# Performance work log

Measured on AMD Instinct MI355X. Metric: run time of the kernel, lower is better.

## Reference

```python
import jax, jax.numpy as jnp
import numpy as np

F_DIM = 32          # phi_feature_dim
P = 128             # preselection_ap (spatial H=W)
NU = 4              # num_users
N1 = NU - 1         # n_cat1 == n_cat2
N3 = (NU - 1) ** 2  # n_cat3


def setup_inputs() -> dict:
    key = jax.random.key(0)
    k1, k2, k3, k4, k5 = jax.random.split(key, 5)
    B, CIN = 32, 8
    phi_input = jax.random.normal(k1, (B, CIN, P, P), dtype=jnp.float32)
    W1 = jax.random.normal(k2, (4 * F_DIM, CIN), dtype=jnp.float32) * 0.1
    b1 = jax.random.normal(k3, (4 * F_DIM,), dtype=jnp.float32) * 0.1
    W3 = jax.random.normal(k4, (4 * F_DIM, 4 * F_DIM), dtype=jnp.float32) * 0.1
    b3 = jax.random.normal(k5, (4 * F_DIM,), dtype=jnp.float32) * 0.1
    ex = jnp.ones((P, P), dtype=jnp.float32) - jnp.eye(P, dtype=jnp.float32)
    return {"phi_input": phi_input, "W1": W1, "b1": b1, "W3": W3, "b3": b3, "ex": ex}


def _conv1x1(x, W, b):
    # 1x1 conv == channel matmul: [b,c,h,w] x [o,c] -> [b,o,h,w]
    return jnp.einsum('bchw,oc->bohw', x, W) + b[None, :, None, None]


def _postprocess(r, ex):
    f = F_DIM
    c0 = r[:, :f]
    c1 = jnp.einsum('ph,bchw->bcpw', ex, r[:, f:2 * f]) / N1
    c2 = jnp.einsum('bchw,wq->bchq', r[:, 2 * f:3 * f], ex) / N1
    c3 = jnp.einsum('ph,bchw,wq->bcpq', ex, r[:, 3 * f:4 * f], ex) / N3
    return jnp.concatenate((c0, c1, c2, c3), axis=1)


def reference(phi_input, W1, b1, W3, b3, ex):
    r = jax.nn.relu(_conv1x1(phi_input, W1, b1))
    r = _postprocess(r, ex)
    r = jax.nn.relu(_conv1x1(r, W3, b3))
    r = _postprocess(r, ex)
    return r
```

## Files before the change

kernel.cpp:

```cpp
#include <hip/hip_runtime.h>
#include <stdint.h>

#define BATCH 32
#define CIN   8
#define NCH   128
#define PP    128
#define NSTRIP 8
#define KSTRIP 16

typedef __attribute__((ext_vector_type(8))) short    bf16x8;
typedef __attribute__((ext_vector_type(4))) float    f32x4;

__device__ __forceinline__ float bf2f(unsigned short u) {
    union { unsigned int i; float f; } x; x.i = ((unsigned int)u) << 16; return x.f;
}
__device__ __forceinline__ unsigned short f2bf(float f) {
    union { float f; unsigned int i; } x; x.f = f;
    unsigned int r = x.i + 0x7fffu + ((x.i >> 16) & 1u);
    return (unsigned short)(r >> 16);
}
__device__ __forceinline__ unsigned int pk2(float a, float b) {
    return (unsigned int)f2bf(a) | ((unsigned int)f2bf(b) << 16);
}

__device__ __forceinline__ int xcd_swz512(int bid) {
    return (bid & 7) * 64 + (bid >> 3);
}

#define SWZB(row, cb) (((row) << 8) + ((cb) ^ (((row) & 7) << 4)))

__global__ __launch_bounds__(512, 4) void k1_sums(const float* __restrict__ phi,
        const float* __restrict__ W1, const float* __restrict__ b1,
        float* __restrict__ RS1t, float* __restrict__ CS1p) {
    __shared__ float cs_f[128 * 132];
    __shared__ unsigned short phi_b[2][1024];
    int bx = blockIdx.x;
    int b = bx >> 3, strip = bx & 7;
    int p0 = strip * 16;
    int tid = threadIdx.x;
    int wv = tid >> 6, l = tid & 63, lr = l & 15, lg = l >> 4;
    int c0 = wv * 16 + lg * 4;

    bf16x8 w1fr = {0, 0, 0, 0, 0, 0, 0, 0};
    if (lg == 0) {
        int cc = wv * 16 + lr;
        float4 wa = *(const float4*)(W1 + cc * 8);
        float4 wb = *(const float4*)(W1 + cc * 8 + 4);
        w1fr[0] = (short)f2bf(wa.x); w1fr[1] = (short)f2bf(wa.y);
        w1fr[2] = (short)f2bf(wa.z); w1fr[3] = (short)f2bf(wa.w);
        w1fr[4] = (short)f2bf(wb.x); w1fr[5] = (short)f2bf(wb.y);
        w1fr[6] = (short)f2bf(wb.z); w1fr[7] = (short)f2bf(wb.w);
    }
    f32x4 binit = {b1[c0], b1[c0 + 1], b1[c0 + 2], b1[c0 + 3]};
    if (tid < 128) {
        bf16x8 pv;
        #pragma unroll
        for (int ci = 0; ci < 8; ++ci)
            pv[ci] = (short)f2bf(phi[((size_t)(b * CIN + ci) * PP + p0) * PP + tid]);
        *(bf16x8*)(phi_b[0] + tid * 8) = pv;
    }
    __syncthreads();

    f32x4 cs_acc[8];
    #pragma unroll
    for (int i = 0; i < 8; ++i) { f32x4 z = {0.f, 0.f, 0.f, 0.f}; cs_acc[i] = z; }

    int cur = 0;
    for (int r = 0; r < 16; ++r) {
        int p = p0 + r;
        float pfv[8];
        if (r < 15 && tid < 128) {
            #pragma unroll
            for (int ci = 0; ci < 8; ++ci)
                pfv[ci] = phi[((size_t)(b * CIN + ci) * PP + p + 1) * PP + tid];
        }
        const unsigned short* pb = phi_b[cur];
        f32x4 rs4 = {0.f, 0.f, 0.f, 0.f};
        #pragma unroll
        for (int pt = 0; pt < 8; ++pt) {
            int pix = pt * 16 + lr;
            bf16x8 bfr1 = {0, 0, 0, 0, 0, 0, 0, 0};
            if (lg == 0) bfr1 = *(const bf16x8*)(pb + pix * 8);
            f32x4 a = __builtin_amdgcn_mfma_f32_16x16x32_bf16(w1fr, bfr1, binit, 0, 0, 0);
            f32x4 v = {fmaxf(a.x, 0.f), fmaxf(a.y, 0.f), fmaxf(a.z, 0.f), fmaxf(a.w, 0.f)};
            cs_acc[pt] += v;
            rs4 += v;
        }
        #pragma unroll
        for (int m = 1; m < 16; m <<= 1) {
            rs4.x += __shfl_xor(rs4.x, m);
            rs4.y += __shfl_xor(rs4.y, m);
            rs4.z += __shfl_xor(rs4.z, m);
            rs4.w += __shfl_xor(rs4.w, m);
        }
        if (lr == 0)
            *(f32x4*)(RS1t + ((size_t)b * PP + p) * NCH + c0) = rs4;
        if (r < 15 && tid < 128) {
            bf16x8 pv;
            #pragma unroll
            for (int ci = 0; ci < 8; ++ci) pv[ci] = (short)f2bf(pfv[ci]);
            *(bf16x8*)(phi_b[cur ^ 1] + tid * 8) = pv;
        }
        __syncthreads();
        cur ^= 1;
    }
    #pragma unroll
    for (int pt = 0; pt < 8; ++pt) {
        f32x4 v = cs_acc[pt];
        int q = pt * 16 + lr;
        cs_f[(c0 + 0) * 132 + q] = v.x;
        cs_f[(c0 + 1) * 132 + q] = v.y;
        cs_f[(c0 + 2) * 132 + q] = v.z;
        cs_f[(c0 + 3) * 132 + q] = v.w;
    }
    __syncthreads();
    float* dstp = CS1p + (size_t)(b * NSTRIP + strip) * NCH * PP;
    for (int k = tid; k < 16384; k += 512) {
        int cc = k >> 7, q = k & 127;
        dstp[k] = cs_f[cc * 132 + q];
    }
}

__global__ __launch_bounds__(256) void k1b_planes(const float* __restrict__ W3,
        const float* __restrict__ b3, const float* __restrict__ RS1t,
        const float* __restrict__ CS1p, float* __restrict__ Ap,
        float* __restrict__ Bqt, unsigned short* __restrict__ W3bf) {
    int bx = blockIdx.x;
    int b = bx >> 2, og = bx & 3;
    int tid = threadIdx.x;
    __shared__ float cs_g[64][132];
    __shared__ float rs_g[64][132];
    __shared__ float s1_96[32];
    for (int k = tid; k < 64 * 128; k += 256) {
        int r = k >> 7, q = k & 127;
        int ch_c = (r < 32) ? (32 + r) : (64 + r);
        float s = 0.f;
        #pragma unroll
        for (int s8 = 0; s8 < NSTRIP; ++s8)
            s += CS1p[((size_t)(b * NSTRIP + s8) * NCH + ch_c) * PP + q];
        cs_g[r][q] = s;
    }
    for (int k = tid; k < 64 * 128; k += 256) {
        int p = k >> 6, r = k & 63;
        rs_g[r][p] = RS1t[((size_t)b * PP + p) * NCH + 64 + r];
    }
    __syncthreads();
    if (tid < 32) {
        float s = 0.f;
        for (int q = 0; q < 128; ++q) s += cs_g[32 + tid][q];
        s1_96[tid] = s;
    }
    int o = og * 32 + (tid >> 3), qh = tid & 7;
    {
        float wa[64];
        #pragma unroll
        for (int r = 0; r < 64; ++r)
            wa[r] = (r < 32) ? W3[o * NCH + 32 + r] * (1.f / 3.f)
                             : -W3[o * NCH + 64 + r] * (1.f / 9.f);
        #pragma unroll
        for (int j = 0; j < 4; ++j) {
            int q = qh * 16 + j * 4;
            float4 a = {0.f, 0.f, 0.f, 0.f};
            #pragma unroll
            for (int r = 0; r < 64; ++r) {
                float4 cv = *(const float4*)&cs_g[r][q];
                a.x = fmaf(wa[r], cv.x, a.x);
                a.y = fmaf(wa[r], cv.y, a.y);
                a.z = fmaf(wa[r], cv.z, a.z);
                a.w = fmaf(wa[r], cv.w, a.w);
            }
            *(float4*)&Ap[((size_t)b * NCH + o) * PP + q] = a;
        }
    }
    __syncthreads();
    float cc = b3[o];
    #pragma unroll
    for (int r = 0; r < 32; ++r)
        cc = fmaf(W3[o * NCH + 96 + r] * (1.f / 9.f), s1_96[r], cc);
    {
        float wb[64];
        #pragma unroll
        for (int r = 0; r < 64; ++r)
            wb[r] = (r < 32) ? W3[o * NCH + 64 + r] * (1.f / 3.f)
                             : -W3[o * NCH + 64 + r] * (1.f / 9.f);
        #pragma unroll
        for (int j = 0; j < 4; ++j) {
            int p4 = qh * 16 + j * 4;
            float4 a = {0.f, 0.f, 0.f, 0.f};
            #pragma unroll
            for (int r = 0; r < 64; ++r) {
                float4 rv = *(const float4*)&rs_g[r][p4];
                a.x = fmaf(wb[r], rv.x, a.x);
                a.y = fmaf(wb[r], rv.y, a.y);
                a.z = fmaf(wb[r], rv.z, a.z);
                a.w = fmaf(wb[r], rv.w, a.w);
            }
            Bqt[((size_t)b * PP + p4 + 0) * NCH + o] = a.x + cc;
            Bqt[((size_t)b * PP + p4 + 1) * NCH + o] = a.y + cc;
            Bqt[((size_t)b * PP + p4 + 2) * NCH + o] = a.z + cc;
            Bqt[((size_t)b * PP + p4 + 3) * NCH + o] = a.w + cc;
        }
    }
    if (bx == 0) {
        for (int i = 0; i < 16; ++i) {
            int k = tid + i * 256;
            float4 w = *(const float4*)(W3 + k * 4);
            int c0 = (k * 4) & 127;
            float sc = (c0 < 32) ? 1.f : ((c0 < 96) ? (-1.f / 3.f) : (1.f / 9.f));
            unsigned int lo = pk2(w.x * sc, w.y * sc);
            unsigned int hi = pk2(w.z * sc, w.w * sc);
            uint2 u = {lo, hi};
            *(uint2*)(W3bf + k * 4) = u;
        }
    }
}

__global__ __launch_bounds__(512) void k2a_sums(const float* __restrict__ phi,
        const float* __restrict__ W1, const float* __restrict__ b1,
        const unsigned short* __restrict__ W3bf,
        const float* __restrict__ Ap, const float* __restrict__ Bqt,
        float* __restrict__ RSvT, float* __restrict__ CSp) {
    int bx = xcd_swz512(blockIdx.x);
    int b = bx >> 4, strip = bx & 15;
    int p0 = strip * 8;
    __shared__ unsigned short w3_l[16384];
    __shared__ unsigned short t_l[16384];
    __shared__ unsigned short phi_b[2][1024];
    __shared__ float BC_l[2][128];
    __shared__ float rs_part[8][64];
    int tid = threadIdx.x;
    int wv = tid >> 6, l = tid & 63, lr = l & 15, lg = l >> 4;
    int q0 = wv * 16 + lg * 4;
    int c0 = q0;

    #pragma unroll
    for (int i = 0; i < 4; ++i) {
        int k = tid + i * 512;
        int o = k >> 4, cb = (k & 15) * 16;
        bf16x8 v = *(const bf16x8*)(W3bf + k * 8);
        *(bf16x8*)((char*)w3_l + SWZB(o, cb)) = v;
    }
    bf16x8 w1fr = {0, 0, 0, 0, 0, 0, 0, 0};
    if (lg == 0) {
        int cc = wv * 16 + lr;
        float4 wa = *(const float4*)(W1 + cc * 8);
        float4 wb = *(const float4*)(W1 + cc * 8 + 4);
        w1fr[0] = (short)f2bf(wa.x); w1fr[1] = (short)f2bf(wa.y);
        w1fr[2] = (short)f2bf(wa.z); w1fr[3] = (short)f2bf(wa.w);
        w1fr[4] = (short)f2bf(wb.x); w1fr[5] = (short)f2bf(wb.y);
        w1fr[6] = (short)f2bf(wb.z); w1fr[7] = (short)f2bf(wb.w);
    }
    f32x4 binit = {b1[c0], b1[c0 + 1], b1[c0 + 2], b1[c0 + 3]};
    f32x4 apr[6];
    #pragma unroll
    for (int nt = 2; nt < 8; ++nt)
        apr[nt - 2] = *(const f32x4*)(Ap + ((size_t)(b * NCH + nt * 16 + lr)) * PP + q0);
    if (tid < 128) {
        bf16x8 pv;
        #pragma unroll
        for (int ci = 0; ci < 8; ++ci)
            pv[ci] = (short)f2bf(phi[((size_t)(b * CIN + ci) * PP + p0) * PP + tid]);
        *(bf16x8*)(phi_b[0] + tid * 8) = pv;
        BC_l[0][tid] = Bqt[((size_t)b * PP + p0) * NCH + tid];
    }
    __syncthreads();

    f32x4 cs1a = {0.f,0.f,0.f,0.f}, cs1b = {0.f,0.f,0.f,0.f};
    f32x4 cs3a = {0.f,0.f,0.f,0.f}, cs3b = {0.f,0.f,0.f,0.f};

    for (int r = 0; r < 8; ++r) {
        int cur = r & 1, nxt = cur ^ 1;
        int p = p0 + r;
        float pfv[8]; float bcn = 0.f;
        if (r < 7 && tid < 128) {
            #pragma unroll
            for (int ci = 0; ci < 8; ++ci)
                pfv[ci] = phi[((size_t)(b * CIN + ci) * PP + p + 1) * PP + tid];
            bcn = Bqt[((size_t)b * PP + p + 1) * NCH + tid];
        }
        const unsigned short* pb = phi_b[cur];
        #pragma unroll
        for (int pt = 0; pt < 8; ++pt) {
            int pix = pt * 16 + lr;
            bf16x8 bfr1 = {0, 0, 0, 0, 0, 0, 0, 0};
            if (lg == 0) bfr1 = *(const bf16x8*)(pb + pix * 8);
            f32x4 a = __builtin_amdgcn_mfma_f32_16x16x32_bf16(w1fr, bfr1, binit, 0, 0, 0);
            uint2 u;
            u.x = pk2(fmaxf(a.x, 0.f), fmaxf(a.y, 0.f));
            u.y = pk2(fmaxf(a.z, 0.f), fmaxf(a.w, 0.f));
            *(uint2*)((char*)t_l + SWZB(pix, c0 * 2)) = u;
        }
        __syncthreads();
        bf16x8 afr[4];
        #pragma unroll
        for (int ks = 0; ks < 4; ++ks)
            afr[ks] = *(const bf16x8*)((char*)t_l + SWZB(wv * 16 + lr, ks * 64 + lg * 16));
        #pragma unroll
        for (int nt = 2; nt < 8; ++nt) {
            int o = nt * 16 + lr;
            bf16x8 bfr[4];
            #pragma unroll
            for (int ks = 0; ks < 4; ++ks)
                bfr[ks] = *(const bf16x8*)((char*)w3_l + SWZB(o, ks * 64 + lg * 16));
            f32x4 acc = apr[nt - 2] + BC_l[cur][o];
            #pragma unroll
            for (int ks = 0; ks < 4; ++ks)
                acc = __builtin_amdgcn_mfma_f32_16x16x32_bf16(afr[ks], bfr[ks], acc, 0, 0, 0);
            f32x4 v = {fmaxf(acc.x, 0.f), fmaxf(acc.y, 0.f), fmaxf(acc.z, 0.f), fmaxf(acc.w, 0.f)};
            if (nt == 2) cs1a += v;
            else if (nt == 3) cs1b += v;
            else if (nt == 6) cs3a += v;
            else if (nt == 7) cs3b += v;
            if (nt >= 4) {
                float rsv = v.x + v.y + v.z + v.w;
                rsv += __shfl_xor(rsv, 16);
                rsv += __shfl_xor(rsv, 32);
                if (lg == 0) rs_part[wv][(nt - 4) * 16 + lr] = rsv;
            }
        }
        if (r < 7 && tid < 128) {
            bf16x8 pv;
            #pragma unroll
            for (int ci = 0; ci < 8; ++ci) pv[ci] = (short)f2bf(pfv[ci]);
            *(bf16x8*)(phi_b[nxt] + tid * 8) = pv;
            BC_l[nxt][tid] = bcn;
        }
        __syncthreads();
        if (tid < 64) {
            float s = 0.f;
            #pragma unroll
            for (int w8 = 0; w8 < 8; ++w8) s += rs_part[w8][tid];
            RSvT[((size_t)(b * PP + p)) * 64 + tid] = s;
        }
    }
    {
        float* dst = CSp + ((size_t)(b * KSTRIP + strip)) * 64 * PP;
        *(f32x4*)(dst + (size_t)(lr)      * PP + q0) = cs1a;
        *(f32x4*)(dst + (size_t)(16 + lr) * PP + q0) = cs1b;
        *(f32x4*)(dst + (size_t)(32 + lr) * PP + q0) = cs3a;
        *(f32x4*)(dst + (size_t)(48 + lr) * PP + q0) = cs3b;
    }
}

__global__ __launch_bounds__(256) void k2s_reduce(const float* __restrict__ CSp,
        const float* __restrict__ RSvT, float* __restrict__ CSv,
        float* __restrict__ Sb) {
    int bx = blockIdx.x;
    int b = bx >> 3, grp = bx & 7;
    int tid = threadIdx.x;
    #pragma unroll
    for (int it = 0; it < 4; ++it) {
        int idx = grp * 1024 + it * 256 + tid;
        float s = 0.f;
        #pragma unroll
        for (int st = 0; st < KSTRIP; ++st)
            s += CSp[((size_t)(b * KSTRIP + st)) * 64 * PP + idx];
        CSv[(size_t)b * 64 * PP + idx] = s;
    }
    if (grp == 0 && tid < 32) {
        float s = 0.f;
        for (int p = 0; p < PP; ++p) s += RSvT[((size_t)(b * PP + p)) * 64 + 32 + tid];
        Sb[b * 32 + tid] = s;
    }
}

__global__ __launch_bounds__(512) void k2b_out(const float* __restrict__ phi,
        const float* __restrict__ W1, const float* __restrict__ b1,
        const unsigned short* __restrict__ W3bf,
        const float* __restrict__ Ap, const float* __restrict__ Bqt,
        const float* __restrict__ RSvT, const float* __restrict__ CSv,
        const float* __restrict__ Sb, float* __restrict__ out) {
    int bx = xcd_swz512(blockIdx.x);
    int b = bx >> 4, strip = bx & 15;
    int p0 = strip * 8;
    __shared__ unsigned short w3_l[16384];
    __shared__ unsigned short t_l[16384];
    __shared__ unsigned short phi_b[2][1024];
    __shared__ float BC_l[2][128];
    __shared__ float rs_row[2][64];
    int tid = threadIdx.x;
    int wv = tid >> 6, l = tid & 63, lr = l & 15, lg = l >> 4;
    int q0 = wv * 16 + lg * 4;
    int c0 = q0;

    #pragma unroll
    for (int i = 0; i < 4; ++i) {
        int k = tid + i * 512;
        int o = k >> 4, cb = (k & 15) * 16;
        bf16x8 v = *(const bf16x8*)(W3bf + k * 8);
        *(bf16x8*)((char*)w3_l + SWZB(o, cb)) = v;
    }
    bf16x8 w1fr = {0, 0, 0, 0, 0, 0, 0, 0};
    if (lg == 0) {
        int cc = wv * 16 + lr;
        float4 wa = *(const float4*)(W1 + cc * 8);
        float4 wb = *(const float4*)(W1 + cc * 8 + 4);
        w1fr[0] = (short)f2bf(wa.x); w1fr[1] = (short)f2bf(wa.y);
        w1fr[2] = (short)f2bf(wa.z); w1fr[3] = (short)f2bf(wa.w);
        w1fr[4] = (short)f2bf(wb.x); w1fr[5] = (short)f2bf(wb.y);
        w1fr[6] = (short)f2bf(wb.z); w1fr[7] = (short)f2bf(wb.w);
    }
    f32x4 binit = {b1[c0], b1[c0 + 1], b1[c0 + 2], b1[c0 + 3]};
    f32x4 apr[8];
    #pragma unroll
    for (int nt = 0; nt < 8; ++nt)
        apr[nt] = *(const f32x4*)(Ap + ((size_t)(b * NCH + nt * 16 + lr)) * PP + q0);
    f32x4 csr[4][2];
    float sjr[4];
    #pragma unroll
    for (int i = 0; i < 4; ++i) {
        int k = tid + i * 512;
        int o = k >> 4, j = k & 15;
        int g = o >> 5;
        f32x4 z = {0.f, 0.f, 0.f, 0.f};
        csr[i][0] = z; csr[i][1] = z; sjr[i] = 0.f;
        if (g == 1) {
            int jc = o - 32;
            csr[i][0] = *(const f32x4*)(CSv + ((size_t)b * 64 + jc) * PP + j * 8);
            csr[i][1] = *(const f32x4*)(CSv + ((size_t)b * 64 + jc) * PP + j * 8 + 4);
        } else if (g == 3) {
            int jc = 32 + (o - 96);
            csr[i][0] = *(const f32x4*)(CSv + ((size_t)b * 64 + jc) * PP + j * 8);
            csr[i][1] = *(const f32x4*)(CSv + ((size_t)b * 64 + jc) * PP + j * 8 + 4);
            sjr[i] = Sb[b * 32 + (o - 96)];
        }
    }
    if (tid < 128) {
        bf16x8 pv;
        #pragma unroll
        for (int ci = 0; ci < 8; ++ci)
            pv[ci] = (short)f2bf(phi[((size_t)(b * CIN + ci) * PP + p0) * PP + tid]);
        *(bf16x8*)(phi_b[0] + tid * 8) = pv;
        BC_l[0][tid] = Bqt[((size_t)b * PP + p0) * NCH + tid];
    } else if (tid < 192) {
        rs_row[0][tid - 128] = RSvT[((size_t)(b * PP + p0)) * 64 + tid - 128];
    }
    __syncthreads();

    for (int r = 0; r < 8; ++r) {
        int cur = r & 1, nxt = cur ^ 1;
        int p = p0 + r;
        float pfv[8]; float bcn = 0.f; float rsn = 0.f;
        if (r < 7) {
            if (tid < 128) {
                #pragma unroll
                for (int ci = 0; ci < 8; ++ci)
                    pfv[ci] = phi[((size_t)(b * CIN + ci) * PP + p + 1) * PP + tid];
                bcn = Bqt[((size_t)b * PP + p + 1) * NCH + tid];
            } else if (tid < 192) {
                rsn = RSvT[((size_t)(b * PP + p + 1)) * 64 + tid - 128];
            }
        }
        const unsigned short* pb = phi_b[cur];
        #pragma unroll
        for (int pt = 0; pt < 8; ++pt) {
            int pix = pt * 16 + lr;
            bf16x8 bfr1 = {0, 0, 0, 0, 0, 0, 0, 0};
            if (lg == 0) bfr1 = *(const bf16x8*)(pb + pix * 8);
            f32x4 a = __builtin_amdgcn_mfma_f32_16x16x32_bf16(w1fr, bfr1, binit, 0, 0, 0);
            uint2 u;
            u.x = pk2(fmaxf(a.x, 0.f), fmaxf(a.y, 0.f));
            u.y = pk2(fmaxf(a.z, 0.f), fmaxf(a.w, 0.f));
            *(uint2*)((char*)t_l + SWZB(pix, c0 * 2)) = u;
        }
        __syncthreads();
        bf16x8 afr[4];
        #pragma unroll
        for (int ks = 0; ks < 4; ++ks)
            afr[ks] = *(const bf16x8*)((char*)t_l + SWZB(wv * 16 + lr, ks * 64 + lg * 16));
        __syncthreads();
        #pragma unroll
        for (int nt = 0; nt < 8; ++nt) {
            int o = nt * 16 + lr;
            bf16x8 bfr[4];
            #pragma unroll
            for (int ks = 0; ks < 4; ++ks)
                bfr[ks] = *(const bf16x8*)((char*)w3_l + SWZB(o, ks * 64 + lg * 16));
            f32x4 acc = apr[nt] + BC_l[cur][o];
            #pragma unroll
            for (int ks = 0; ks < 4; ++ks)
                acc = __builtin_amdgcn_mfma_f32_16x16x32_bf16(afr[ks], bfr[ks], acc, 0, 0, 0);
            uint2 u;
            u.x = pk2(fmaxf(acc.x, 0.f), fmaxf(acc.y, 0.f));
            u.y = pk2(fmaxf(acc.z, 0.f), fmaxf(acc.w, 0.f));
            *(uint2*)((char*)t_l + SWZB(o, q0 * 2)) = u;
        }
        if (r < 7) {
            if (tid < 128) {
                bf16x8 pv;
                #pragma unroll
                for (int ci = 0; ci < 8; ++ci) pv[ci] = (short)f2bf(pfv[ci]);
                *(bf16x8*)(phi_b[nxt] + tid * 8) = pv;
                BC_l[nxt][tid] = bcn;
            } else if (tid < 192) {
                rs_row[nxt][tid - 128] = rsn;
            }
        }
        __syncthreads();
        #pragma unroll
        for (int i = 0; i < 4; ++i) {
            int k = tid + i * 512;
            int o = k >> 4, j = k & 15;
            int g = o >> 5;
            bf16x8 u = *(const bf16x8*)((char*)t_l + SWZB(o, j * 16));
            float rp = (g >= 2) ? rs_row[cur][o - 64] : 0.f;
            float o8[8];
            #pragma unroll
            for (int e = 0; e < 8; ++e) {
                float v = bf2f((unsigned short)u[e]);
                float cq = (e < 4) ? ((const float*)&csr[i][0])[e]
                                   : ((const float*)&csr[i][1])[e - 4];
                float rr;
                if (g == 0)      rr = v;
                else if (g == 1) rr = (cq - v) * (1.f / 3.f);
                else if (g == 2) rr = (rp - v) * (1.f / 3.f);
                else             rr = ((sjr[i] - rp) - cq + v) * (1.f / 9.f);
                o8[e] = rr;
            }
            f32x4 lo = {o8[0], o8[1], o8[2], o8[3]};
            f32x4 hi = {o8[4], o8[5], o8[6], o8[7]};
            float* dst = out + ((size_t)(b * NCH + o) * PP + p) * PP + j * 8;
            *(f32x4*)dst       = lo;
            *(f32x4*)(dst + 4) = hi;
        }
        __syncthreads();
    }
}

extern "C" void kernel_launch(void* const* d_in, const int* in_sizes, int n_in,
                              void* d_out, int out_size, void* d_ws, size_t ws_size,
                              hipStream_t stream) {
    (void)in_sizes; (void)n_in; (void)out_size; (void)ws_size;
    const float* phi = (const float*)d_in[0];
    const float* W1  = (const float*)d_in[1];
    const float* b1  = (const float*)d_in[2];
    const float* W3  = (const float*)d_in[3];
    const float* b3  = (const float*)d_in[4];
    float* out = (float*)d_out;

    char* ws = (char*)d_ws;
    size_t off = 0;
    float* RS1t = (float*)(ws + off); off += (size_t)BATCH * NCH * PP * 4;
    float* CS1p = (float*)(ws + off); off += (size_t)BATCH * NSTRIP * NCH * PP * 4;
    float* Ap   = (float*)(ws + off); off += (size_t)BATCH * NCH * PP * 4;
    float* Bqt  = (float*)(ws + off); off += (size_t)BATCH * NCH * PP * 4;
    unsigned short* W3bf = (unsigned short*)(ws + off); off += (size_t)NCH * NCH * 2;
    float* RSvT = (float*)(ws + off); off += (size_t)BATCH * PP * 64 * 4;
    float* CSp  = (float*)(ws + off); off += (size_t)BATCH * KSTRIP * 64 * PP * 4;
    float* CSv  = (float*)(ws + off); off += (size_t)BATCH * 64 * PP * 4;
    float* Sb   = (float*)(ws + off); off += (size_t)BATCH * 32 * 4;

    k1_sums<<<BATCH * NSTRIP, 512, 0, stream>>>(phi, W1, b1, RS1t, CS1p);
    k1b_planes<<<BATCH * 4, 256, 0, stream>>>(W3, b3, RS1t, CS1p, Ap, Bqt, W3bf);
    k2a_sums<<<BATCH * KSTRIP, 512, 0, stream>>>(phi, W1, b1, W3bf, Ap, Bqt, RSvT, CSp);
    k2s_reduce<<<BATCH * 8, 256, 0, stream>>>(CSp, RSvT, CSv, Sb);
    k2b_out<<<BATCH * KSTRIP, 512, 0, stream>>>(phi, W1, b1, W3bf, Ap, Bqt, RSvT, CSv, Sb, out);
}
```

Baseline: 187.0 us.

## Replace partial-sum buffer and reduce kernel with atomic accumulation

Removes the k2s_reduce launch and the per-strip CSp partial buffer. k2a_sums now atomically adds its column-sum partials straight into CSv and its row sums into Sb, and k1_sums zeroes those buffers first. This saves a kernel launch and a write-then-read of the partial buffer. In exchange it adds many scalar float atomics, which may contend, and makes the summation order nondeterministic.

```diff
diff --git a/kernel.cpp b/kernel.cpp
--- a/kernel.cpp
+++ b/kernel.cpp
@@ -31,7 +31,8 @@
 
 __global__ __launch_bounds__(512, 4) void k1_sums(const float* __restrict__ phi,
         const float* __restrict__ W1, const float* __restrict__ b1,
-        float* __restrict__ RS1t, float* __restrict__ CS1p) {
+        float* __restrict__ RS1t, float* __restrict__ CS1p,
+        float* __restrict__ CSv, float* __restrict__ Sb) {
     __shared__ float cs_f[128 * 132];
     __shared__ unsigned short phi_b[2][1024];
     int bx = blockIdx.x;
@@ -40,6 +41,9 @@
     int tid = threadIdx.x;
     int wv = tid >> 6, l = tid & 63, lr = l & 15, lg = l >> 4;
     int c0 = wv * 16 + lg * 4;
+
+    *(float2*)(CSv + (size_t)bx * 1024 + tid * 2) = (float2){0.f, 0.f};
+    if (bx < 2) Sb[bx * 512 + tid] = 0.f;
 
     bf16x8 w1fr = {0, 0, 0, 0, 0, 0, 0, 0};
     if (lg == 0) {
@@ -219,7 +223,8 @@
         const float* __restrict__ W1, const float* __restrict__ b1,
         const unsigned short* __restrict__ W3bf,
         const float* __restrict__ Ap, const float* __restrict__ Bqt,
-        float* __restrict__ RSvT, float* __restrict__ CSp) {
+        float* __restrict__ RSvT, float* __restrict__ CSv,
+        float* __restrict__ Sb) {
     int bx = xcd_swz512(blockIdx.x);
     int b = bx >> 4, strip = bx & 15;
     int p0 = strip * 8;
@@ -331,36 +336,18 @@
             #pragma unroll
             for (int w8 = 0; w8 < 8; ++w8) s += rs_part[w8][tid];
             RSvT[((size_t)(b * PP + p)) * 64 + tid] = s;
+            if (tid >= 32) atomicAdd(&Sb[b * 32 + tid - 32], s);
         }
     }
     {
-        float* dst = CSp + ((size_t)(b * KSTRIP + strip)) * 64 * PP;
-        *(f32x4*)(dst + (size_t)(lr)      * PP + q0) = cs1a;
-        *(f32x4*)(dst + (size_t)(16 + lr) * PP + q0) = cs1b;
-        *(f32x4*)(dst + (size_t)(32 + lr) * PP + q0) = cs3a;
-        *(f32x4*)(dst + (size_t)(48 + lr) * PP + q0) = cs3b;
-    }
-}
-
-__global__ __launch_bounds__(256) void k2s_reduce(const float* __restrict__ CSp,
-        const float* __restrict__ RSvT, float* __restrict__ CSv,
-        float* __restrict__ Sb) {
-    int bx = blockIdx.x;
-    int b = bx >> 3, grp = bx & 7;
-    int tid = threadIdx.x;
-    #pragma unroll
-    for (int it = 0; it < 4; ++it) {
-        int idx = grp * 1024 + it * 256 + tid;
-        float s = 0.f;
-        #pragma unroll
-        for (int st = 0; st < KSTRIP; ++st)
-            s += CSp[((size_t)(b * KSTRIP + st)) * 64 * PP + idx];
-        CSv[(size_t)b * 64 * PP + idx] = s;
-    }
-    if (grp == 0 && tid < 32) {
-        float s = 0.f;
-        for (int p = 0; p < PP; ++p) s += RSvT[((size_t)(b * PP + p)) * 64 + 32 + tid];
-        Sb[b * 32 + tid] = s;
+        float* dst = CSv + (size_t)b * 64 * PP;
+        #pragma unroll
+        for (int e = 0; e < 4; ++e) {
+            atomicAdd(dst + (size_t)(lr)      * PP + q0 + e, ((const float*)&cs1a)[e]);
+            atomicAdd(dst + (size_t)(16 + lr) * PP + q0 + e, ((const float*)&cs1b)[e]);
+            atomicAdd(dst + (size_t)(32 + lr) * PP + q0 + e, ((const float*)&cs3a)[e]);
+            atomicAdd(dst + (size_t)(48 + lr) * PP + q0 + e, ((const float*)&cs3b)[e]);
+        }
     }
 }
 
@@ -546,13 +533,11 @@
     float* Bqt  = (float*)(ws + off); off += (size_t)BATCH * NCH * PP * 4;
     unsigned short* W3bf = (unsigned short*)(ws + off); off += (size_t)NCH * NCH * 2;
     float* RSvT = (float*)(ws + off); off += (size_t)BATCH * PP * 64 * 4;
-    float* CSp  = (float*)(ws + off); off += (size_t)BATCH * KSTRIP * 64 * PP * 4;
     float* CSv  = (float*)(ws + off); off += (size_t)BATCH * 64 * PP * 4;
     float* Sb   = (float*)(ws + off); off += (size_t)BATCH * 32 * 4;
 
-    k1_sums<<<BATCH * NSTRIP, 512, 0, stream>>>(phi, W1, b1, RS1t, CS1p);
+    k1_sums<<<BATCH * NSTRIP, 512, 0, stream>>>(phi, W1, b1, RS1t, CS1p, CSv, Sb);
     k1b_planes<<<BATCH * 4, 256, 0, stream>>>(W3, b3, RS1t, CS1p, Ap, Bqt, W3bf);
-    k2a_sums<<<BATCH * KSTRIP, 512, 0, stream>>>(phi, W1, b1, W3bf, Ap, Bqt, RSvT, CSp);
-    k2s_reduce<<<BATCH * 8, 256, 0, stream>>>(CSp, RSvT, CSv, Sb);
+    k2a_sums<<<BATCH * KSTRIP, 512, 0, stream>>>(phi, W1, b1, W3bf, Ap, Bqt, RSvT, CSv, Sb);
     k2b_out<<<BATCH * KSTRIP, 512, 0, stream>>>(phi, W1, b1, W3bf, Ap, Bqt, RSvT, CSv, Sb, out);
 }
```

Result: slower. 226.3 us (+21.0%).
